# Kernel tuning notes

Hardware: AMD Instinct MI355X
Metric: run time of the kernel (lower is better)

The kernel has to match this reference:

```python
import jax, jax.numpy as jnp
import numpy as np

RADIUS = 0.05      # outer ball-query radius
MIN_RADIUS = 0.02  # inner exclusion radius


def setup_inputs() -> dict:
    key = jax.random.key(0)
    k1, k2 = jax.random.split(key)
    # raw layout is [B, C, N, 1] as consumed by forward's squeeze(-1).permute(0,2,1)
    xyz = jax.random.uniform(k1, (4, 3, 4096, 1), dtype=jnp.float32)      # coords in unit cube
    points = jax.random.normal(k2, (4, 64, 4096, 1), dtype=jnp.float32)   # per-point features
    return {"xyz": xyz, "points": points}


def _pairwise_sqdist(x):
    # x: [B, N, 3] -> [B, N, N] squared euclidean distances
    sq = jnp.sum(x * x, axis=-1)  # [B, N]
    return sq[:, :, None] + sq[:, None, :] - 2.0 * jnp.einsum('bnc,bmc->bnm', x, x)


def reference(xyz, points):
    # [B, C, N, 1] -> [B, N, C]
    _xyz = jnp.transpose(xyz[..., 0], (0, 2, 1))       # [B, N, 3]
    _points = jnp.transpose(points[..., 0], (0, 2, 1))  # [B, N, D]
    B, N, C = _xyz.shape

    # downsample_query_ball: ball-query neighbor counts in annulus (min_radius, radius),
    # keep the N//2 densest points
    d2 = _pairwise_sqdist(_xyz)                              # [B, N, N]
    nbr_cnt = jnp.sum(((d2 < RADIUS ** 2) & (d2 > MIN_RADIUS ** 2)).astype(jnp.int32), axis=-1)
    _, idx = jax.lax.top_k(nbr_cnt, N // 2)                  # [B, N//2]

    # index_points: gather along the point axis
    new_xyz = jnp.take_along_axis(_xyz, idx[..., None], axis=1)        # [B, N//2, 3]
    new_points = jnp.take_along_axis(_points, idx[..., None], axis=1)  # [B, N//2, D]
    return new_xyz, new_points
```

## Files before the change

kernel.cpp:

```cpp
#include <hip/hip_runtime.h>


#pragma clang fp contract(off)

#define BN 4
#define NPTS 4096
#define ND 64
#define KSEL 2048
#define R2 0.0025f
#define M2 0.0004f

#define IPT 4
#define ITILES 4
#define JC 32
#define JCH 128
#define JP (JCH / 2)

typedef float f32x2 __attribute__((ext_vector_type(2)));

__global__ __launch_bounds__(256) void count_part_kernel(
        const float* __restrict__ xyz, unsigned short* __restrict__ part) {
    __shared__ float4 sA[JP];
    __shared__ float4 sB[JP];
    const int jc = blockIdx.x & (JC - 1);
    const int it = (blockIdx.x >> 5) & (ITILES - 1);
    const int b  = blockIdx.x >> 7;
    const float* base = xyz + (size_t)b * 3 * NPTS;

    if (threadIdx.x < JP) {
        int j0 = jc * JCH + 2 * threadIdx.x;
        float2 xv = *(const float2*)(base + j0);
        float2 yv = *(const float2*)(base + NPTS + j0);
        float2 zv = *(const float2*)(base + 2 * NPTS + j0);
        float sq0 = __fadd_rn(__fadd_rn(__fmul_rn(xv.x, xv.x),
                                        __fmul_rn(yv.x, yv.x)),
                              __fmul_rn(zv.x, zv.x));
        float sq1 = __fadd_rn(__fadd_rn(__fmul_rn(xv.y, xv.y),
                                        __fmul_rn(yv.y, yv.y)),
                              __fmul_rn(zv.y, zv.y));
        sA[threadIdx.x] = make_float4(xv.x, xv.y, yv.x, yv.y);
        sB[threadIdx.x] = make_float4(zv.x, zv.y, sq0, sq1);
    }
    const int ibase = it * 1024 + threadIdx.x;
    f32x2 mx[IPT], my[IPT], mz[IPT], ms[IPT];
    #pragma unroll
    for (int k = 0; k < IPT; ++k) {
        int i = ibase + k * 256;
        float x = base[i], y = base[NPTS + i], z = base[2 * NPTS + i];
        float sq = __fadd_rn(__fadd_rn(__fmul_rn(x, x), __fmul_rn(y, y)),
                             __fmul_rn(z, z));
        mx[k] = (f32x2){x, x};  my[k] = (f32x2){y, y};
        mz[k] = (f32x2){z, z};  ms[k] = (f32x2){sq, sq};
    }
    __syncthreads();

    const int      m2i1  = __float_as_int(M2) + 1;
    const unsigned range = (unsigned)(__float_as_int(R2) - __float_as_int(M2)) - 1u;

    int cnt[IPT] = {0, 0, 0, 0};
    const f32x2 two2 = {2.0f, 2.0f};
    #pragma unroll 2
    for (int jp = 0; jp < JP; ++jp) {
        float4 A = sA[jp], B = sB[jp];
        f32x2 px = {A.x, A.y}, py = {A.z, A.w};
        f32x2 pz = {B.x, B.y}, pw = {B.z, B.w};
        #pragma unroll
        for (int k = 0; k < IPT; ++k) {
            f32x2 t0  = mx[k] * px;
            f32x2 t1  = my[k] * py;
            f32x2 t2  = mz[k] * pz;
            f32x2 dot = (t0 + t1) + t2;
            f32x2 d2  = (ms[k] + pw) - two2 * dot;
            cnt[k] += ((unsigned)(__float_as_int(d2.x) - m2i1) < range) ? 1 : 0;
            cnt[k] += ((unsigned)(__float_as_int(d2.y) - m2i1) < range) ? 1 : 0;
        }
    }
    unsigned short* pp = part + (size_t)((b * ITILES + it) * JC + jc) * 1024;
    #pragma unroll
    for (int k = 0; k < IPT; ++k)
        pp[threadIdx.x + k * 256] = (unsigned short)cnt[k];
}

__global__ __launch_bounds__(256) void rank_gather_kernel(
        const float* __restrict__ xyz, const float* __restrict__ points,
        const unsigned short* __restrict__ part, float* __restrict__ out) {
    __shared__ union {
        alignas(16) int skey[NPTS];
        float sfeat[ND][68];
    } sh;
    __shared__ int spr[4][64];
    __shared__ int srank[64];
    const int b     = blockIdx.x >> 6;
    const int tbase = (blockIdx.x & 63) * 64;
    const int tid   = threadIdx.x;

    {
        const unsigned short* pbase = part + (size_t)b * ITILES * JC * 1024;
        #pragma unroll
        for (int gg = 0; gg < 2; ++gg) {
            const int g    = tid + gg * 256;
            const int it   = g >> 7;
            const int loc8 = (g & 127) * 8;
            const int4* pp =
                (const int4*)(pbase + (size_t)it * JC * 1024 + loc8);
            int4 s = make_int4(0, 0, 0, 0);
            #pragma unroll 8
            for (int jc = 0; jc < JC; ++jc) {
                int4 v = pp[jc * 128];
                s.x += v.x; s.y += v.y; s.z += v.z; s.w += v.w;
            }
            const int i0 = it * 1024 + loc8;
            int4 ka, kb;
            ka.x = ((s.x & 0xFFFF) << 12)          | (NPTS - 1 - (i0 + 0));
            ka.y = (((unsigned)s.x >> 16) << 12)   | (NPTS - 1 - (i0 + 1));
            ka.z = ((s.y & 0xFFFF) << 12)          | (NPTS - 1 - (i0 + 2));
            ka.w = (((unsigned)s.y >> 16) << 12)   | (NPTS - 1 - (i0 + 3));
            kb.x = ((s.z & 0xFFFF) << 12)          | (NPTS - 1 - (i0 + 4));
            kb.y = (((unsigned)s.z >> 16) << 12)   | (NPTS - 1 - (i0 + 5));
            kb.z = ((s.w & 0xFFFF) << 12)          | (NPTS - 1 - (i0 + 6));
            kb.w = (((unsigned)s.w >> 16) << 12)   | (NPTS - 1 - (i0 + 7));
            ((int4*)sh.skey)[g * 2]     = ka;
            ((int4*)sh.skey)[g * 2 + 1] = kb;
        }
    }
    __syncthreads();

    {
        const int pi = tid & 63;
        const int q  = tid >> 6;
        const int ki = sh.skey[tbase + pi];
        const int4* sk4 = (const int4*)sh.skey;
        int r = 0;
        #pragma unroll 8
        for (int jj = q * 256; jj < q * 256 + 256; ++jj) {
            int4 v = sk4[jj];
            r += (v.x > ki) ? 1 : 0;
            r += (v.y > ki) ? 1 : 0;
            r += (v.z > ki) ? 1 : 0;
            r += (v.w > ki) ? 1 : 0;
        }
        spr[q][pi] = r;
    }
    __syncthreads();

    if (tid < 64) {
        const int rank = spr[0][tid] + spr[1][tid] + spr[2][tid] + spr[3][tid];
        srank[tid] = rank;
        const int i = tbase + tid;
        if (rank < KSEL) {
            const float* xb = xyz + (size_t)b * 3 * NPTS;
            float* o = out + ((size_t)b * KSEL + rank) * 3;
            o[0] = xb[i]; o[1] = xb[NPTS + i]; o[2] = xb[2 * NPTS + i];
        }
    }
    __syncthreads();

    {
        const int ii = tid & 63;
        const int q  = tid >> 6;
        #pragma unroll
        for (int r16 = 0; r16 < 16; ++r16) {
            const int c = q + 4 * r16;
            sh.sfeat[c][ii] = points[((size_t)b * ND + c) * NPTS + tbase + ii];
        }
    }
    __syncthreads();

    {
        const int pt = tid >> 2;
        const int c4 = tid & 3;
        const int rank = srank[pt];
        if (rank < KSEL) {
            float* orow = out + (size_t)BN * KSEL * 3 +
                          ((size_t)b * KSEL + rank) * ND;
            #pragma unroll
            for (int u4 = 0; u4 < 4; ++u4) {
                const int c0 = u4 * 16 + c4 * 4;
                float4 v = make_float4(sh.sfeat[c0 + 0][pt],
                                       sh.sfeat[c0 + 1][pt],
                                       sh.sfeat[c0 + 2][pt],
                                       sh.sfeat[c0 + 3][pt]);
                *(float4*)(orow + c0) = v;
            }
        }
    }
}

extern "C" void kernel_launch(void* const* d_in, const int* in_sizes, int n_in,
                              void* d_out, int out_size, void* d_ws, size_t ws_size,
                              hipStream_t stream) {
    const float* xyz    = (const float*)d_in[0];
    const float* points = (const float*)d_in[1];
    float* out = (float*)d_out;
    unsigned short* part = (unsigned short*)d_ws;

    count_part_kernel<<<BN * ITILES * JC, 256, 0, stream>>>(xyz, part);
    rank_gather_kernel<<<BN * 64, 256, 0, stream>>>(xyz, points, part, out);
}
```

Baseline: 85.91 us.

## Store partial neighbor counts as point-major bytes and reduce with udot4

The partial annulus counts per 128-point column chunk are now stored as one byte per chunk, in a point-major layout, instead of 16-bit values in chunk-major tiles. This halves the workspace traffic. It also lets the rank kernel read each point's 32 partials contiguously and sum them with byte dot-product instructions. Separately, the distance expression is rewritten to use a fused multiply-add for the -2*dot term. That cuts one operation per pair in the hot loop, but it changes the rounding compared with the non-contracted reference and can flip counts for pairs right at the radius boundaries. The byte stores in the count kernel are now strided by 32 bytes, which makes the writes less coalesced.

New measurement: 85.45 us. No clear change (-0.5%).

```diff
diff --git a/kernel.cpp b/kernel.cpp
--- a/kernel.cpp
+++ b/kernel.cpp
@@ -18,8 +18,32 @@
 
 typedef float f32x2 __attribute__((ext_vector_type(2)));
 
+#if __has_builtin(__builtin_amdgcn_udot4)
+#define BYTESUM4(v, acc) __builtin_amdgcn_udot4((unsigned)(v), 0x01010101u, (acc), false)
+#else
+static __device__ __forceinline__ unsigned BYTESUM4(unsigned v, unsigned acc) {
+    return acc + (v & 0xFFu) + ((v >> 8) & 0xFFu) + ((v >> 16) & 0xFFu) + (v >> 24);
+}
+#endif
+#define SUM16(a, b, c)                                                        \
+    BYTESUM4((unsigned)(b).w, BYTESUM4((unsigned)(b).z,                       \
+    BYTESUM4((unsigned)(b).y, BYTESUM4((unsigned)(b).x,                       \
+    BYTESUM4((unsigned)(a).w, BYTESUM4((unsigned)(a).z,                       \
+    BYTESUM4((unsigned)(a).y, BYTESUM4((unsigned)(a).x, (c)))))))))
+
+static __device__ __forceinline__ f32x2 fma2(f32x2 a, f32x2 b, f32x2 c) {
+#if __has_builtin(__builtin_elementwise_fma)
+    return __builtin_elementwise_fma(a, b, c);
+#else
+    f32x2 r;
+    r.x = __builtin_fmaf(a.x, b.x, c.x);
+    r.y = __builtin_fmaf(a.y, b.y, c.y);
+    return r;
+#endif
+}
+
 __global__ __launch_bounds__(256) void count_part_kernel(
-        const float* __restrict__ xyz, unsigned short* __restrict__ part) {
+        const float* __restrict__ xyz, unsigned char* __restrict__ part) {
     __shared__ float4 sA[JP];
     __shared__ float4 sB[JP];
     const int jc = blockIdx.x & (JC - 1);
@@ -58,7 +82,7 @@
     const unsigned range = (unsigned)(__float_as_int(R2) - __float_as_int(M2)) - 1u;
 
     int cnt[IPT] = {0, 0, 0, 0};
-    const f32x2 two2 = {2.0f, 2.0f};
+    const f32x2 ntwo2 = {-2.0f, -2.0f};
     #pragma unroll 2
     for (int jp = 0; jp < JP; ++jp) {
         float4 A = sA[jp], B = sB[jp];
@@ -70,20 +94,21 @@
             f32x2 t1  = my[k] * py;
             f32x2 t2  = mz[k] * pz;
             f32x2 dot = (t0 + t1) + t2;
-            f32x2 d2  = (ms[k] + pw) - two2 * dot;
+            f32x2 spw = ms[k] + pw;
+            f32x2 d2  = fma2(dot, ntwo2, spw);
             cnt[k] += ((unsigned)(__float_as_int(d2.x) - m2i1) < range) ? 1 : 0;
             cnt[k] += ((unsigned)(__float_as_int(d2.y) - m2i1) < range) ? 1 : 0;
         }
     }
-    unsigned short* pp = part + (size_t)((b * ITILES + it) * JC + jc) * 1024;
+    unsigned char* pb = part + (size_t)b * NPTS * JC + jc;
     #pragma unroll
     for (int k = 0; k < IPT; ++k)
-        pp[threadIdx.x + k * 256] = (unsigned short)cnt[k];
+        pb[(size_t)(ibase + k * 256) * JC] = (unsigned char)cnt[k];
 }
 
 __global__ __launch_bounds__(256) void rank_gather_kernel(
         const float* __restrict__ xyz, const float* __restrict__ points,
-        const unsigned short* __restrict__ part, float* __restrict__ out) {
+        const unsigned char* __restrict__ part, float* __restrict__ out) {
     __shared__ union {
         alignas(16) int skey[NPTS];
         float sfeat[ND][68];
@@ -95,32 +120,23 @@
     const int tid   = threadIdx.x;
 
     {
-        const unsigned short* pbase = part + (size_t)b * ITILES * JC * 1024;
+        const unsigned char* pbase = part + (size_t)b * NPTS * JC;
         #pragma unroll
-        for (int gg = 0; gg < 2; ++gg) {
-            const int g    = tid + gg * 256;
-            const int it   = g >> 7;
-            const int loc8 = (g & 127) * 8;
-            const int4* pp =
-                (const int4*)(pbase + (size_t)it * JC * 1024 + loc8);
-            int4 s = make_int4(0, 0, 0, 0);
-            #pragma unroll 8
-            for (int jc = 0; jc < JC; ++jc) {
-                int4 v = pp[jc * 128];
-                s.x += v.x; s.y += v.y; s.z += v.z; s.w += v.w;
-            }
-            const int i0 = it * 1024 + loc8;
-            int4 ka, kb;
-            ka.x = ((s.x & 0xFFFF) << 12)          | (NPTS - 1 - (i0 + 0));
-            ka.y = (((unsigned)s.x >> 16) << 12)   | (NPTS - 1 - (i0 + 1));
-            ka.z = ((s.y & 0xFFFF) << 12)          | (NPTS - 1 - (i0 + 2));
-            ka.w = (((unsigned)s.y >> 16) << 12)   | (NPTS - 1 - (i0 + 3));
-            kb.x = ((s.z & 0xFFFF) << 12)          | (NPTS - 1 - (i0 + 4));
-            kb.y = (((unsigned)s.z >> 16) << 12)   | (NPTS - 1 - (i0 + 5));
-            kb.z = ((s.w & 0xFFFF) << 12)          | (NPTS - 1 - (i0 + 6));
-            kb.w = (((unsigned)s.w >> 16) << 12)   | (NPTS - 1 - (i0 + 7));
-            ((int4*)sh.skey)[g * 2]     = ka;
-            ((int4*)sh.skey)[g * 2 + 1] = kb;
+        for (int r = 0; r < 4; ++r) {
+            const int p4 = r * 1024 + tid * 4;
+            const int4* q = (const int4*)(pbase + (size_t)p4 * JC);
+            int4 w0 = q[0], w1 = q[1], w2 = q[2], w3 = q[3];
+            int4 w4 = q[4], w5 = q[5], w6 = q[6], w7 = q[7];
+            unsigned c0 = SUM16(w0, w1, 0u);
+            unsigned c1 = SUM16(w2, w3, 0u);
+            unsigned c2 = SUM16(w4, w5, 0u);
+            unsigned c3 = SUM16(w6, w7, 0u);
+            int4 ka;
+            ka.x = (int)(c0 << 12) | (NPTS - 1 - (p4 + 0));
+            ka.y = (int)(c1 << 12) | (NPTS - 1 - (p4 + 1));
+            ka.z = (int)(c2 << 12) | (NPTS - 1 - (p4 + 2));
+            ka.w = (int)(c3 << 12) | (NPTS - 1 - (p4 + 3));
+            ((int4*)sh.skey)[r * 256 + tid] = ka;
         }
     }
     __syncthreads();
@@ -192,7 +208,7 @@
     const float* xyz    = (const float*)d_in[0];
     const float* points = (const float*)d_in[1];
     float* out = (float*)d_out;
-    unsigned short* part = (unsigned short*)d_ws;
+    unsigned char* part = (unsigned char*)d_ws;
 
     count_part_kernel<<<BN * ITILES * JC, 256, 0, stream>>>(xyz, part);
     rank_gather_kernel<<<BN * 64, 256, 0, stream>>>(xyz, points, part, out);
```

## Replace brute-force pairwise counting with uniform-grid cell binning

Applied to the files above, without the earlier changes.

Swaps the all-pairs O(N^2) distance count for a 16^3 uniform grid. A per-batch binning kernel counting-sorts points by cell, and a second kernel counts annulus neighbours only among the 3x3x3 adjacent cells, split across three z-slices per point. The rank kernel then sums the three partial counts and scatters them back to original indices through the sort permutation. This cuts the arithmetic work a great deal but adds an extra launch, a single-block-per-batch binning step with shared atomics, and divergent variable-length inner loops.

Measured after the change: 78.43 us. 8.7% less time.

```diff
diff --git a/kernel.cpp b/kernel.cpp
--- a/kernel.cpp
+++ b/kernel.cpp
@@ -9,81 +9,123 @@
 #define KSEL 2048
 #define R2 0.0025f
 #define M2 0.0004f
-
-#define IPT 4
-#define ITILES 4
-#define JC 32
-#define JCH 128
-#define JP (JCH / 2)
-
-typedef float f32x2 __attribute__((ext_vector_type(2)));
-
-__global__ __launch_bounds__(256) void count_part_kernel(
-        const float* __restrict__ xyz, unsigned short* __restrict__ part) {
-    __shared__ float4 sA[JP];
-    __shared__ float4 sB[JP];
-    const int jc = blockIdx.x & (JC - 1);
-    const int it = (blockIdx.x >> 5) & (ITILES - 1);
-    const int b  = blockIdx.x >> 7;
+#define NCELL 4096
+#define CS_STRIDE 4100
+
+typedef unsigned int u32;
+typedef unsigned short u16;
+
+#define OFF_SORTED 0
+#define OFF_SIDX   262144
+#define OFF_CS     294912
+#define OFF_PART   360512
+
+__global__ __launch_bounds__(1024) void bin_kernel(
+        const float* __restrict__ xyz, float4* __restrict__ sorted,
+        u16* __restrict__ sidx, u32* __restrict__ cellstart) {
+    __shared__ u32 hist[NCELL];
+    __shared__ u32 wtot[16];
+    const int b = blockIdx.x;
     const float* base = xyz + (size_t)b * 3 * NPTS;
-
-    if (threadIdx.x < JP) {
-        int j0 = jc * JCH + 2 * threadIdx.x;
-        float2 xv = *(const float2*)(base + j0);
-        float2 yv = *(const float2*)(base + NPTS + j0);
-        float2 zv = *(const float2*)(base + 2 * NPTS + j0);
-        float sq0 = __fadd_rn(__fadd_rn(__fmul_rn(xv.x, xv.x),
-                                        __fmul_rn(yv.x, yv.x)),
-                              __fmul_rn(zv.x, zv.x));
-        float sq1 = __fadd_rn(__fadd_rn(__fmul_rn(xv.y, xv.y),
-                                        __fmul_rn(yv.y, yv.y)),
-                              __fmul_rn(zv.y, zv.y));
-        sA[threadIdx.x] = make_float4(xv.x, xv.y, yv.x, yv.y);
-        sB[threadIdx.x] = make_float4(zv.x, zv.y, sq0, sq1);
-    }
-    const int ibase = it * 1024 + threadIdx.x;
-    f32x2 mx[IPT], my[IPT], mz[IPT], ms[IPT];
-    #pragma unroll
-    for (int k = 0; k < IPT; ++k) {
-        int i = ibase + k * 256;
+    const int tid = threadIdx.x;
+    for (int k = tid; k < NCELL; k += 1024) hist[k] = 0u;
+    __syncthreads();
+
+    u32 crk[4];
+    #pragma unroll
+    for (int k = 0; k < 4; ++k) {
+        const int i = tid + k * 1024;
+        float x = base[i], y = base[NPTS + i], z = base[2 * NPTS + i];
+        int c = (int)(x * 16.0f) | ((int)(y * 16.0f) << 4)
+                                 | ((int)(z * 16.0f) << 8);
+        u32 r = atomicAdd(&hist[c], 1u);
+        crk[k] = ((u32)c << 16) | r;
+    }
+    __syncthreads();
+
+    u32 v4[4], sum = 0;
+    #pragma unroll
+    for (int k = 0; k < 4; ++k) { v4[k] = hist[tid * 4 + k]; sum += v4[k]; }
+    const int lane = tid & 63, w = tid >> 6;
+    u32 incl = sum;
+    #pragma unroll
+    for (int d = 1; d < 64; d <<= 1) {
+        u32 t = __shfl_up(incl, d, 64);
+        if (lane >= d) incl += t;
+    }
+    if (lane == 63) wtot[w] = incl;
+    __syncthreads();
+    u32 woff = 0;
+    #pragma unroll
+    for (int ww = 0; ww < 16; ++ww) woff += (ww < w) ? wtot[ww] : 0u;
+    u32 run = woff + incl - sum;
+    #pragma unroll
+    for (int k = 0; k < 4; ++k) { u32 h = v4[k]; hist[tid * 4 + k] = run; run += h; }
+    __syncthreads();
+
+    u32* csb = cellstart + b * CS_STRIDE;
+    #pragma unroll
+    for (int k = 0; k < 4; ++k) {
+        const int i = tid + k * 1024;
         float x = base[i], y = base[NPTS + i], z = base[2 * NPTS + i];
         float sq = __fadd_rn(__fadd_rn(__fmul_rn(x, x), __fmul_rn(y, y)),
                              __fmul_rn(z, z));
-        mx[k] = (f32x2){x, x};  my[k] = (f32x2){y, y};
-        mz[k] = (f32x2){z, z};  ms[k] = (f32x2){sq, sq};
-    }
-    __syncthreads();
+        u32 c = crk[k] >> 16, r = crk[k] & 0xFFFFu;
+        u32 pos = hist[c] + r;
+        sorted[((size_t)b << 12) + pos] = make_float4(x, y, z, sq);
+        sidx[((size_t)b << 12) + pos]   = (u16)i;
+    }
+    for (int k = tid; k < NCELL; k += 1024) csb[k] = hist[k];
+    if (tid == 0) csb[NCELL] = NPTS;
+}
+
+__global__ __launch_bounds__(256) void count_grid_kernel(
+        const float4* __restrict__ sorted, const u32* __restrict__ cellstart,
+        u16* __restrict__ part3) {
+    const int g  = blockIdx.x * 256 + threadIdx.x;
+    const int b  = g / (3 * NPTS);
+    const int rg = g - b * 3 * NPTS;
+    const int dz = rg >> 12;
+    const int p  = rg & (NPTS - 1);
+
+    const float4* sb = sorted + ((size_t)b << 12);
+    const float4 v = sb[p];
+    const int cx = (int)(v.x * 16.0f);
+    const int cy = (int)(v.y * 16.0f);
+    const int cz = (int)(v.z * 16.0f);
+    const int zz = cz + dz - 1;
 
     const int      m2i1  = __float_as_int(M2) + 1;
     const unsigned range = (unsigned)(__float_as_int(R2) - __float_as_int(M2)) - 1u;
 
-    int cnt[IPT] = {0, 0, 0, 0};
-    const f32x2 two2 = {2.0f, 2.0f};
-    #pragma unroll 2
-    for (int jp = 0; jp < JP; ++jp) {
-        float4 A = sA[jp], B = sB[jp];
-        f32x2 px = {A.x, A.y}, py = {A.z, A.w};
-        f32x2 pz = {B.x, B.y}, pw = {B.z, B.w};
-        #pragma unroll
-        for (int k = 0; k < IPT; ++k) {
-            f32x2 t0  = mx[k] * px;
-            f32x2 t1  = my[k] * py;
-            f32x2 t2  = mz[k] * pz;
-            f32x2 dot = (t0 + t1) + t2;
-            f32x2 d2  = (ms[k] + pw) - two2 * dot;
-            cnt[k] += ((unsigned)(__float_as_int(d2.x) - m2i1) < range) ? 1 : 0;
-            cnt[k] += ((unsigned)(__float_as_int(d2.y) - m2i1) < range) ? 1 : 0;
-        }
-    }
-    unsigned short* pp = part + (size_t)((b * ITILES + it) * JC + jc) * 1024;
-    #pragma unroll
-    for (int k = 0; k < IPT; ++k)
-        pp[threadIdx.x + k * 256] = (unsigned short)cnt[k];
+    u32 cnt = 0;
+    if ((unsigned)zz < 16u) {
+        const u32* cs = cellstart + b * CS_STRIDE + (zz << 8);
+        const int x0  = (cx > 0)  ? cx - 1 : 0;
+        const int x1e = ((cx < 15) ? cx + 1 : 15) + 1;
+        const int y0  = (cy > 0)  ? cy - 1 : 0;
+        const int y1  = (cy < 15) ? cy + 1 : 15;
+        for (int y = y0; y <= y1; ++y) {
+            u32 s = cs[(y << 4) + x0];
+            u32 e = cs[(y << 4) + x1e];
+            for (u32 q = s; q < e; ++q) {
+                float4 u = sb[q];
+                float dot = __fadd_rn(__fadd_rn(__fmul_rn(v.x, u.x),
+                                                __fmul_rn(v.y, u.y)),
+                                      __fmul_rn(v.z, u.z));
+                float spw = __fadd_rn(v.w, u.w);
+                float d2  = __builtin_fmaf(dot, -2.0f, spw);
+                cnt += ((unsigned)(__float_as_int(d2) - m2i1) < range) ? 1u : 0u;
+            }
+        }
+    }
+    part3[((size_t)((b << 12) | p) << 2) + dz] = (u16)cnt;
 }
 
 __global__ __launch_bounds__(256) void rank_gather_kernel(
         const float* __restrict__ xyz, const float* __restrict__ points,
-        const unsigned short* __restrict__ part, float* __restrict__ out) {
+        const u16* __restrict__ part3, const u16* __restrict__ sidx,
+        float* __restrict__ out) {
     __shared__ union {
         alignas(16) int skey[NPTS];
         float sfeat[ND][68];
@@ -95,32 +137,18 @@
     const int tid   = threadIdx.x;
 
     {
-        const unsigned short* pbase = part + (size_t)b * ITILES * JC * 1024;
+        const uint4* pq = (const uint4*)(part3 + ((size_t)b << 12) * 4);
+        const u32*   sx = (const u32*)(sidx + ((size_t)b << 12));
         #pragma unroll
-        for (int gg = 0; gg < 2; ++gg) {
-            const int g    = tid + gg * 256;
-            const int it   = g >> 7;
-            const int loc8 = (g & 127) * 8;
-            const int4* pp =
-                (const int4*)(pbase + (size_t)it * JC * 1024 + loc8);
-            int4 s = make_int4(0, 0, 0, 0);
-            #pragma unroll 8
-            for (int jc = 0; jc < JC; ++jc) {
-                int4 v = pp[jc * 128];
-                s.x += v.x; s.y += v.y; s.z += v.z; s.w += v.w;
-            }
-            const int i0 = it * 1024 + loc8;
-            int4 ka, kb;
-            ka.x = ((s.x & 0xFFFF) << 12)          | (NPTS - 1 - (i0 + 0));
-            ka.y = (((unsigned)s.x >> 16) << 12)   | (NPTS - 1 - (i0 + 1));
-            ka.z = ((s.y & 0xFFFF) << 12)          | (NPTS - 1 - (i0 + 2));
-            ka.w = (((unsigned)s.y >> 16) << 12)   | (NPTS - 1 - (i0 + 3));
-            kb.x = ((s.z & 0xFFFF) << 12)          | (NPTS - 1 - (i0 + 4));
-            kb.y = (((unsigned)s.z >> 16) << 12)   | (NPTS - 1 - (i0 + 5));
-            kb.z = ((s.w & 0xFFFF) << 12)          | (NPTS - 1 - (i0 + 6));
-            kb.w = (((unsigned)s.w >> 16) << 12)   | (NPTS - 1 - (i0 + 7));
-            ((int4*)sh.skey)[g * 2]     = ka;
-            ((int4*)sh.skey)[g * 2 + 1] = kb;
+        for (int r = 0; r < 8; ++r) {
+            const int gp = r * 256 + tid;
+            uint4 q = pq[gp];
+            u32  od = sx[gp];
+            u32 c0 = (q.x & 0xFFFFu) + (q.x >> 16) + (q.y & 0xFFFFu);
+            u32 c1 = (q.z & 0xFFFFu) + (q.z >> 16) + (q.w & 0xFFFFu);
+            int o0 = (int)(od & 0xFFFFu), o1 = (int)(od >> 16);
+            sh.skey[o0] = (int)(c0 << 12) | (NPTS - 1 - o0);
+            sh.skey[o1] = (int)(c1 << 12) | (NPTS - 1 - o1);
         }
     }
     __syncthreads();
@@ -192,8 +220,14 @@
     const float* xyz    = (const float*)d_in[0];
     const float* points = (const float*)d_in[1];
     float* out = (float*)d_out;
-    unsigned short* part = (unsigned short*)d_ws;
-
-    count_part_kernel<<<BN * ITILES * JC, 256, 0, stream>>>(xyz, part);
-    rank_gather_kernel<<<BN * 64, 256, 0, stream>>>(xyz, points, part, out);
-}
+    char*  ws  = (char*)d_ws;
+
+    float4* sorted   = (float4*)(ws + OFF_SORTED);
+    u16*    sidx     = (u16*)  (ws + OFF_SIDX);
+    u32*    cellstart= (u32*)  (ws + OFF_CS);
+    u16*    part3    = (u16*)  (ws + OFF_PART);
+
+    bin_kernel       <<<BN, 1024, 0, stream>>>(xyz, sorted, sidx, cellstart);
+    count_grid_kernel<<<BN * 3 * NPTS / 256, 256, 0, stream>>>(sorted, cellstart, part3);
+    rank_gather_kernel<<<BN * 64, 256, 0, stream>>>(xyz, points, part3, sidx, out);
+}
```
